# Kernel tuning notes

Measured on AMD Instinct MI355X. Metric: run time of the kernel, lower is better.

Reference implementation:

```python
import jax, jax.numpy as jnp
import numpy as np

B, S, D, H = 4, 1024, 1024, 16
DK = D // H


def setup_inputs() -> dict:
    key = jax.random.key(0)
    ks = jax.random.split(key, 12)
    scale = 1.0 / np.sqrt(D)
    inp = {
        'Q': jax.random.normal(ks[0], (B, S, D), jnp.float32),
        'K': jax.random.normal(ks[1], (B, S, D), jnp.float32),
        'V': jax.random.normal(ks[2], (B, S, D), jnp.float32),
        'mask': jnp.tril(jnp.ones((S, S), bool))[None, None],  # [1,1,S,S] causal
        'Wq': jax.random.normal(ks[3], (D, D), jnp.float32) * scale,
        'bq': jnp.zeros((D,), jnp.float32),
        'Wk': jax.random.normal(ks[4], (D, D), jnp.float32) * scale,
        'bk': jnp.zeros((D,), jnp.float32),
        'Wv': jax.random.normal(ks[5], (D, D), jnp.float32) * scale,
        'bv': jnp.zeros((D,), jnp.float32),
        'Wo': jax.random.normal(ks[6], (D, D), jnp.float32) * scale,
        'bo': jnp.zeros((D,), jnp.float32),
    }
    return inp


def reference(Q, K, V, mask, Wq, bq, Wk, bk, Wv, bv, Wo, bo):
    # Linear projections (torch Linear: x @ W.T + b)
    q = Q @ Wq.T + bq
    k = K @ Wk.T + bk
    v = V @ Wv.T + bv
    # [B,S,D] -> [B,H,S,DK]
    q = q.reshape(B, S, H, DK).transpose(0, 2, 1, 3)
    k = k.reshape(B, S, H, DK).transpose(0, 2, 1, 3)
    v = v.reshape(B, S, H, DK).transpose(0, 2, 1, 3)
    scores = jnp.einsum('bhqd,bhkd->bhqk', q, k) / jnp.sqrt(jnp.float32(DK))
    scores = jnp.where(mask, scores, jnp.float32(-1e9))
    attn = jax.nn.softmax(scores, axis=-1)
    x = jnp.einsum('bhqk,bhkd->bhqd', attn, v)
    x = x.transpose(0, 2, 1, 3).reshape(B, S, D)
    out = x @ Wo.T + bo
    return out, attn
```

## Files before the change

### kernel.cpp

```cpp
#include <hip/hip_runtime.h>
#include <hip/hip_bf16.h>
#include <cstdint>

#define NB 4
#define NS 1024
#define ND 1024
#define NH 16
#define NDK 64
#define NBH 64

typedef unsigned short u16;
typedef __attribute__((ext_vector_type(8))) short short8;
typedef __attribute__((ext_vector_type(4))) float f32x4;
typedef __attribute__((ext_vector_type(4))) unsigned short u16x4;

#define SWZ(r, c) ((c) ^ (((r) & 7) << 3))

__device__ __forceinline__ u16 f2bf(float x) {
  unsigned u = __builtin_bit_cast(unsigned, x);
  return (u16)((u + 0x7fffu + ((u >> 16) & 1u)) >> 16);
}
__device__ __forceinline__ float bf2f(u16 b) {
  return __builtin_bit_cast(float, ((unsigned)b) << 16);
}

__device__ __forceinline__ void async16(u16* lds_dst, const u16* gsrc) {
  __builtin_amdgcn_global_load_lds(
      (const __attribute__((address_space(1))) void*)gsrc,
      (__attribute__((address_space(3))) void*)lds_dst, 16, 0, 0);
}

struct CvtArgs {
  const float* src[7];
  u16* dst[7];
  int n4[7];
};

__global__ __launch_bounds__(256) void cvt_k(CvtArgs a) {
  const int seg = blockIdx.y;
  const float* s = a.src[seg];
  u16* d = a.dst[seg];
  const int n4 = a.n4[seg];
  for (int i = blockIdx.x * 256 + threadIdx.x; i < n4; i += gridDim.x * 256) {
    float4 v = *(const float4*)&s[(size_t)i * 4];
    u16x4 pk = {f2bf(v.x), f2bf(v.y), f2bf(v.z), f2bf(v.w)};
    *(u16x4*)&d[(size_t)i * 4] = pk;
  }
}

template <int KTILES, int LDA, int LDB>
__device__ __forceinline__ void gemm_bt_core(const u16* __restrict__ A,
                                             const u16* __restrict__ BT,
                                             u16* As, u16* Bs, f32x4 (&acc)[4][4],
                                             int bm0, int bn0, int wave, int lane) {
  const int lrow = lane & 15;
  const int lkg = lane >> 4;
  const int wm = wave >> 1, wn = wave & 1;
#pragma unroll 1
  for (int t = 0; t < KTILES; ++t) {
    const int k0 = t * 64;
#pragma unroll
    for (int j = 0; j < 4; ++j) {
      const int c = (wave * 4 + j) * 64 + lane;
      const int row = c >> 3;
      const int gc = (c & 7) ^ (row & 7);
      async16(&As[(wave * 4 + j) * 512], A + (size_t)(bm0 + row) * LDA + k0 + gc * 8);
      async16(&Bs[(wave * 4 + j) * 512], BT + (size_t)(bn0 + row) * LDB + k0 + gc * 8);
    }
    asm volatile("s_waitcnt vmcnt(0)" ::: "memory");
    __syncthreads();
#pragma unroll
    for (int kk = 0; kk < 2; ++kk) {
      short8 av[4], bv[4];
#pragma unroll
      for (int i = 0; i < 4; ++i) {
        const int r = wm * 64 + i * 16 + lrow;
        av[i] = *(const short8*)&As[r * 64 + SWZ(r, kk * 32 + lkg * 8)];
      }
#pragma unroll
      for (int j = 0; j < 4; ++j) {
        const int r = wn * 64 + j * 16 + lrow;
        bv[j] = *(const short8*)&Bs[r * 64 + SWZ(r, kk * 32 + lkg * 8)];
      }
#pragma unroll
      for (int i = 0; i < 4; ++i)
#pragma unroll
        for (int j = 0; j < 4; ++j)
          acc[i][j] = __builtin_amdgcn_mfma_f32_16x16x32_bf16(av[i], bv[j], acc[i][j], 0, 0, 0);
    }
    __syncthreads();
  }
}

struct ProjArgs {
  const u16* A[3];
  const u16* W[3];
  const float* bias[3];
  u16* dst[3];
};

__global__ __launch_bounds__(256, 3) void proj_gemm(ProjArgs pa) {
  const int z = blockIdx.z;
  const u16* A = pa.A[z];
  const u16* BT = pa.W[z];
  const float* bias = pa.bias[z];
  u16* dst = pa.dst[z];

  __shared__ u16 As[128 * 64];
  __shared__ u16 Bs[128 * 64];
  const int tid = threadIdx.x, wave = tid >> 6, lane = tid & 63;
  const int lrow = lane & 15, lkg = lane >> 4;
  const int wm = wave >> 1, wn = wave & 1;
  const int bm0 = blockIdx.x * 128, bn0 = blockIdx.y * 128;

  f32x4 acc[4][4] = {};
  gemm_bt_core<16, ND, ND>(A, BT, As, Bs, acc, bm0, bn0, wave, lane);

#pragma unroll
  for (int i = 0; i < 4; ++i) {
#pragma unroll
    for (int j = 0; j < 4; ++j) {
      const int m0 = bm0 + wm * 64 + i * 16 + lkg * 4;
      const int n = bn0 + wn * 64 + j * 16 + lrow;
      const float bn_ = bias[n];
      const int b = m0 >> 10;
      const int h = n >> 6, dk = n & 63;
      if (z < 2) {
#pragma unroll
        for (int r = 0; r < 4; ++r) {
          const int s = (m0 + r) & 1023;
          dst[(((size_t)(b * NH + h)) * NS + s) * NDK + dk] = f2bf(acc[i][j][r] + bn_);
        }
      } else {
        const int s0 = m0 & 1023;
        u16x4 pk;
#pragma unroll
        for (int r = 0; r < 4; ++r) pk[r] = f2bf(acc[i][j][r] + bn_);
        *(u16x4*)&dst[(((size_t)(b * NH + h)) * NDK + dk) * NS + s0] = pk;
      }
    }
  }
}

__global__ __launch_bounds__(512, 2) void attn_fused(
    const u16* __restrict__ qh, const u16* __restrict__ kh,
    const u16* __restrict__ vT, float* __restrict__ attn,
    u16* __restrict__ xh) {
  __shared__ __align__(16) char smem_raw[81920];
  u16* sc = (u16*)smem_raw;
  u16* kb = (u16*)(smem_raw + 65536);
  float* m_sub = (float*)(smem_raw + 65536);
  float* m_final = (float*)(smem_raw + 65536 + 512);

  const int tid = threadIdx.x;
  const int wave = tid >> 6, lane = tid & 63;
  const int lrow = lane & 15, lkg = lane >> 4;
  const int qs = wave >> 2, ks = wave & 3;

  const int flat = (int)blockIdx.x;
  const int r8 = flat & 7;
  const int inner = flat >> 3;
  const int strip = inner & 31;
  const int bh = r8 + 8 * (inner >> 5);
  const int mt = 31 - strip;

  const int s0 = mt * 32;
  const int nkt = (mt >> 1) + 1;
  const int nk = nkt * 64;
  const u16* Qb = qh + (size_t)bh * NS * NDK;
  const u16* Kb = kh + (size_t)bh * NS * NDK;
  const u16* Vb = vT + (size_t)bh * NS * NDK;
  float* attn_s = attn + (size_t)bh * NS * NS + (size_t)s0 * NS;

  auto stage8k = [&](u16* buf, const u16* src, int ld) {
    const int row = tid >> 3, scol = tid & 7;
    const int gc = scol ^ (row & 7);
    async16(buf + wave * 512, src + (size_t)row * ld + gc * 8);
  };

  if (tid < 256) {
    const int row = tid >> 3, scol = tid & 7;
    const int gc = scol ^ (row & 7);
    async16(kb + 4096 + wave * 512, Qb + (size_t)(s0 + row) * NDK + gc * 8);
  }
  asm volatile("s_waitcnt vmcnt(0)" ::: "memory");
  __syncthreads();
  short8 qv[2];
  {
    const int q = qs * 16 + lrow;
#pragma unroll
    for (int kk = 0; kk < 2; ++kk)
      qv[kk] = *(const short8*)&kb[4096 + q * 64 + SWZ(q, kk * 32 + lkg * 8)];
  }
  __syncthreads();

  float m_run = -3e38f;
  stage8k(kb, Kb, NDK);
#pragma unroll 1
  for (int t = 0; t < nkt; ++t) {
    const bool have_next = (t + 1 < nkt);
    if (have_next) stage8k(kb + ((t + 1) & 1) * 4096, Kb + (size_t)(t + 1) * 64 * NDK, NDK);
    if (have_next) asm volatile("s_waitcnt vmcnt(1)" ::: "memory");
    else           asm volatile("s_waitcnt vmcnt(0)" ::: "memory");
    __builtin_amdgcn_s_barrier();
    const u16* kbuf = kb + (t & 1) * 4096;
    const int krow = ks * 16 + lrow;
    f32x4 acc = {};
#pragma unroll
    for (int kk = 0; kk < 2; ++kk) {
      short8 av = *(const short8*)&kbuf[krow * 64 + SWZ(krow, kk * 32 + lkg * 8)];
      acc = __builtin_amdgcn_mfma_f32_16x16x32_bf16(av, qv[kk], acc, 0, 0, 0);
    }
    const int qloc = qs * 16 + lrow;
    const int qg = s0 + qloc;
    u16x4 pk;
#pragma unroll
    for (int r = 0; r < 4; ++r) {
      float s = acc[r] * 0.125f;
      const int kg = t * 64 + ks * 16 + lkg * 4 + r;
      if (kg > qg) s = -1e30f;
      m_run = fmaxf(m_run, s);
      pk[r] = f2bf(s);
    }
    *(u16x4*)&sc[qloc * 1024 + SWZ(qloc, t * 64 + ks * 16 + lkg * 4)] = pk;
    __builtin_amdgcn_s_barrier();
  }
  __syncthreads();

  m_run = fmaxf(m_run, __shfl_xor(m_run, 16, 64));
  m_run = fmaxf(m_run, __shfl_xor(m_run, 32, 64));
  if (lane < 16) m_sub[wave * 16 + lane] = m_run;
  __syncthreads();
  if (tid < 32) {
    const int qq = tid >> 4, r = tid & 15;
    float m = m_sub[(qq * 4 + 0) * 16 + r];
    m = fmaxf(m, m_sub[(qq * 4 + 1) * 16 + r]);
    m = fmaxf(m, m_sub[(qq * 4 + 2) * 16 + r]);
    m = fmaxf(m, m_sub[(qq * 4 + 3) * 16 + r]);
    m_final[tid] = m;
  }
  __syncthreads();

#pragma unroll 1
  for (int rr = 0; rr < 4; ++rr) {
    const int q = wave * 4 + rr;
    const float m = m_final[q];
    float part = 0.f;
#pragma unroll 1
    for (int c0 = 0; c0 < nk; c0 += 256) {
      const int c = c0 + lane * 4;
      if (c < nk) {
        u16x4 e4 = *(u16x4*)&sc[q * 1024 + SWZ(q, c)];
        u16x4 pk;
#pragma unroll
        for (int e = 0; e < 4; ++e) {
          const float pe = __expf(bf2f(e4[e]) - m);
          part += pe;
          pk[e] = f2bf(pe);
        }
        *(u16x4*)&sc[q * 1024 + SWZ(q, c)] = pk;
      }
    }
#pragma unroll
    for (int o = 32; o; o >>= 1) part += __shfl_xor(part, o, 64);
    const float inv = 1.0f / part;
#pragma unroll 1
    for (int c0 = 0; c0 < NS; c0 += 256) {
      const int c = c0 + lane * 4;
      f32x4 o4 = {0.f, 0.f, 0.f, 0.f};
      if (c < nk) {
        u16x4 e4 = *(u16x4*)&sc[q * 1024 + SWZ(q, c)];
        u16x4 pn;
#pragma unroll
        for (int e = 0; e < 4; ++e) {
          const float pe = bf2f(e4[e]) * inv;
          o4[e] = pe;
          pn[e] = f2bf(pe);
        }
        *(u16x4*)&sc[q * 1024 + SWZ(q, c)] = pn;
      }
      __builtin_nontemporal_store(o4, (f32x4*)&attn_s[(size_t)q * NS + c]);
    }
  }
  __syncthreads();

  f32x4 xacc = {};
  stage8k(kb, Vb, NS);
#pragma unroll 1
  for (int t = 0; t < nkt; ++t) {
    const bool have_next = (t + 1 < nkt);
    if (have_next) stage8k(kb + ((t + 1) & 1) * 4096, Vb + (size_t)(t + 1) * 64, NS);
    if (have_next) asm volatile("s_waitcnt vmcnt(1)" ::: "memory");
    else           asm volatile("s_waitcnt vmcnt(0)" ::: "memory");
    __builtin_amdgcn_s_barrier();
    const u16* vbuf = kb + (t & 1) * 4096;
    const int qrow = qs * 16 + lrow;
    const int vrow = ks * 16 + lrow;
#pragma unroll
    for (int kk = 0; kk < 2; ++kk) {
      short8 av = *(const short8*)&sc[qrow * 1024 + SWZ(qrow, t * 64 + kk * 32 + lkg * 8)];
      short8 bv = *(const short8*)&vbuf[vrow * 64 + SWZ(vrow, kk * 32 + lkg * 8)];
      xacc = __builtin_amdgcn_mfma_f32_16x16x32_bf16(av, bv, xacc, 0, 0, 0);
    }
    __builtin_amdgcn_s_barrier();
  }

  {
    const int b = bh >> 4, h = bh & 15;
    const int dk = ks * 16 + lrow;
#pragma unroll
    for (int r = 0; r < 4; ++r) {
      const int q = qs * 16 + lkg * 4 + r;
      xh[(size_t)(b * NS + s0 + q) * ND + h * NDK + dk] = f2bf(xacc[r]);
    }
  }
}

__global__ __launch_bounds__(256, 3) void out_gemm(const u16* __restrict__ xh,
                                                   const u16* __restrict__ Wo,
                                                   const float* __restrict__ bo,
                                                   float* __restrict__ out) {
  __shared__ u16 As[128 * 64];
  __shared__ u16 Bs[128 * 64];
  const int tid = threadIdx.x, wave = tid >> 6, lane = tid & 63;
  const int lrow = lane & 15, lkg = lane >> 4;
  const int wm = wave >> 1, wn = wave & 1;
  const int bm0 = blockIdx.x * 128, bn0 = blockIdx.y * 128;

  f32x4 acc[4][4] = {};
  gemm_bt_core<16, ND, ND>(xh, Wo, As, Bs, acc, bm0, bn0, wave, lane);

#pragma unroll
  for (int i = 0; i < 4; ++i) {
#pragma unroll
    for (int j = 0; j < 4; ++j) {
      const int m0 = bm0 + wm * 64 + i * 16 + lkg * 4;
      const int n = bn0 + wn * 64 + j * 16 + lrow;
      const float bn_ = bo[n];
#pragma unroll
      for (int r = 0; r < 4; ++r)
        out[(size_t)(m0 + r) * ND + n] = acc[i][j][r] + bn_;
    }
  }
}

extern "C" void kernel_launch(void* const* d_in, const int* in_sizes, int n_in,
                              void* d_out, int out_size, void* d_ws, size_t ws_size,
                              hipStream_t stream) {
  const float* Q = (const float*)d_in[0];
  const float* K = (const float*)d_in[1];
  const float* V = (const float*)d_in[2];
  const float* Wq = (const float*)d_in[4];
  const float* bq = (const float*)d_in[5];
  const float* Wk = (const float*)d_in[6];
  const float* bk = (const float*)d_in[7];
  const float* Wv = (const float*)d_in[8];
  const float* bv = (const float*)d_in[9];
  const float* Wo = (const float*)d_in[10];
  const float* bo = (const float*)d_in[11];

  char* ws = (char*)d_ws;
  const size_t MB = 1u << 20;
  u16* Wq_b = (u16*)(ws + 0 * MB);
  u16* Wk_b = (u16*)(ws + 2 * MB);
  u16* Wv_b = (u16*)(ws + 4 * MB);
  u16* Wo_b = (u16*)(ws + 6 * MB);
  u16* Qb   = (u16*)(ws + 8 * MB);
  u16* Kb   = (u16*)(ws + 16 * MB);
  u16* Vb   = (u16*)(ws + 24 * MB);
  u16* qh   = (u16*)(ws + 32 * MB);
  u16* kh   = (u16*)(ws + 40 * MB);
  u16* vT   = (u16*)(ws + 48 * MB);
  u16* xh   = (u16*)(ws + 56 * MB);

  float* out = (float*)d_out;
  float* attn = out + (size_t)NB * NS * ND;

  CvtArgs ca;
  ca.src[0] = Q;  ca.dst[0] = Qb;   ca.n4[0] = (NB * NS * ND) / 4;
  ca.src[1] = K;  ca.dst[1] = Kb;   ca.n4[1] = (NB * NS * ND) / 4;
  ca.src[2] = V;  ca.dst[2] = Vb;   ca.n4[2] = (NB * NS * ND) / 4;
  ca.src[3] = Wq; ca.dst[3] = Wq_b; ca.n4[3] = (ND * ND) / 4;
  ca.src[4] = Wk; ca.dst[4] = Wk_b; ca.n4[4] = (ND * ND) / 4;
  ca.src[5] = Wv; ca.dst[5] = Wv_b; ca.n4[5] = (ND * ND) / 4;
  ca.src[6] = Wo; ca.dst[6] = Wo_b; ca.n4[6] = (ND * ND) / 4;
  cvt_k<<<dim3(512, 7), 256, 0, stream>>>(ca);

  ProjArgs pa;
  pa.A[0] = Qb; pa.W[0] = Wq_b; pa.bias[0] = bq; pa.dst[0] = qh;
  pa.A[1] = Kb; pa.W[1] = Wk_b; pa.bias[1] = bk; pa.dst[1] = kh;
  pa.A[2] = Vb; pa.W[2] = Wv_b; pa.bias[2] = bv; pa.dst[2] = vT;
  proj_gemm<<<dim3((NB * NS) / 128, ND / 128, 3), 256, 0, stream>>>(pa);

  attn_fused<<<dim3(32 * NBH), 512, 0, stream>>>(qh, kh, vT, attn, xh);

  out_gemm<<<dim3((NB * NS) / 128, ND / 128), 256, 0, stream>>>(xh, Wo_b, bo, out);
}
```

Baseline: 134.1 us.

## Double-buffer output GEMM and defer softmax normalization to the PV epilogue

Adds a double-buffered GEMM core that prefetches the next K tile with async loads while computing the current one, and uses it in the output projection, reducing occupancy to two blocks per CU. In attention, the second softmax pass no longer rewrites normalized probabilities back to shared memory. The unnormalized exponentials feed the P·V MFMA, and the per-row reciprocal is stored in shared memory and applied to the accumulator before the bf16 store. This trades a write pass over the score buffer, plus one extra barrier, for a small rounding difference because bf16 rounding now happens before normalization.

```diff
diff --git a/kernel.cpp b/kernel.cpp
--- a/kernel.cpp
+++ b/kernel.cpp
@@ -92,6 +92,59 @@
   }
 }
 
+template <int KTILES, int LDA, int LDB>
+__device__ __forceinline__ void gemm_bt_db(const u16* __restrict__ A,
+                                           const u16* __restrict__ BT,
+                                           u16 (&As)[2][128 * 64], u16 (&Bs)[2][128 * 64],
+                                           f32x4 (&acc)[4][4],
+                                           int bm0, int bn0, int wave, int lane) {
+  const int lrow = lane & 15;
+  const int lkg = lane >> 4;
+  const int wm = wave >> 1, wn = wave & 1;
+  auto stage = [&](int buf, int t) {
+    const int k0 = t * 64;
+#pragma unroll
+    for (int j = 0; j < 4; ++j) {
+      const int c = (wave * 4 + j) * 64 + lane;
+      const int row = c >> 3;
+      const int gc = (c & 7) ^ (row & 7);
+      async16(&As[buf][(wave * 4 + j) * 512], A + (size_t)(bm0 + row) * LDA + k0 + gc * 8);
+      async16(&Bs[buf][(wave * 4 + j) * 512], BT + (size_t)(bn0 + row) * LDB + k0 + gc * 8);
+    }
+  };
+  stage(0, 0);
+#pragma unroll 1
+  for (int t = 0; t < KTILES; ++t) {
+    const bool have_next = (t + 1 < KTILES);
+    if (have_next) stage((t + 1) & 1, t + 1);
+    if (have_next) asm volatile("s_waitcnt vmcnt(8)" ::: "memory");
+    else           asm volatile("s_waitcnt vmcnt(0)" ::: "memory");
+    __builtin_amdgcn_s_barrier();
+    const u16* as = As[t & 1];
+    const u16* bs = Bs[t & 1];
+#pragma unroll
+    for (int kk = 0; kk < 2; ++kk) {
+      short8 av[4], bv[4];
+#pragma unroll
+      for (int i = 0; i < 4; ++i) {
+        const int r = wm * 64 + i * 16 + lrow;
+        av[i] = *(const short8*)&as[r * 64 + SWZ(r, kk * 32 + lkg * 8)];
+      }
+#pragma unroll
+      for (int j = 0; j < 4; ++j) {
+        const int r = wn * 64 + j * 16 + lrow;
+        bv[j] = *(const short8*)&bs[r * 64 + SWZ(r, kk * 32 + lkg * 8)];
+      }
+#pragma unroll
+      for (int i = 0; i < 4; ++i)
+#pragma unroll
+        for (int j = 0; j < 4; ++j)
+          acc[i][j] = __builtin_amdgcn_mfma_f32_16x16x32_bf16(av[i], bv[j], acc[i][j], 0, 0, 0);
+    }
+    __builtin_amdgcn_s_barrier();
+  }
+}
+
 struct ProjArgs {
   const u16* A[3];
   const u16* W[3];
@@ -151,6 +204,7 @@
   u16* kb = (u16*)(smem_raw + 65536);
   float* m_sub = (float*)(smem_raw + 65536);
   float* m_final = (float*)(smem_raw + 65536 + 512);
+  float* s_inv = (float*)(smem_raw + 65536 + 768);
 
   const int tid = threadIdx.x;
   const int wave = tid >> 6, lane = tid & 63;
@@ -264,24 +318,24 @@
 #pragma unroll
     for (int o = 32; o; o >>= 1) part += __shfl_xor(part, o, 64);
     const float inv = 1.0f / part;
+    if (lane == 0) s_inv[q] = inv;
 #pragma unroll 1
     for (int c0 = 0; c0 < NS; c0 += 256) {
       const int c = c0 + lane * 4;
       f32x4 o4 = {0.f, 0.f, 0.f, 0.f};
       if (c < nk) {
         u16x4 e4 = *(u16x4*)&sc[q * 1024 + SWZ(q, c)];
-        u16x4 pn;
-#pragma unroll
-        for (int e = 0; e < 4; ++e) {
-          const float pe = bf2f(e4[e]) * inv;
-          o4[e] = pe;
-          pn[e] = f2bf(pe);
-        }
-        *(u16x4*)&sc[q * 1024 + SWZ(q, c)] = pn;
+#pragma unroll
+        for (int e = 0; e < 4; ++e) o4[e] = bf2f(e4[e]) * inv;
       }
       __builtin_nontemporal_store(o4, (f32x4*)&attn_s[(size_t)q * NS + c]);
     }
   }
+  __syncthreads();
+
+  f32x4 inv4;
+#pragma unroll
+  for (int r = 0; r < 4; ++r) inv4[r] = s_inv[qs * 16 + lkg * 4 + r];
   __syncthreads();
 
   f32x4 xacc = {};
@@ -311,24 +365,24 @@
 #pragma unroll
     for (int r = 0; r < 4; ++r) {
       const int q = qs * 16 + lkg * 4 + r;
-      xh[(size_t)(b * NS + s0 + q) * ND + h * NDK + dk] = f2bf(xacc[r]);
-    }
-  }
-}
-
-__global__ __launch_bounds__(256, 3) void out_gemm(const u16* __restrict__ xh,
+      xh[(size_t)(b * NS + s0 + q) * ND + h * NDK + dk] = f2bf(xacc[r] * inv4[r]);
+    }
+  }
+}
+
+__global__ __launch_bounds__(256, 2) void out_gemm(const u16* __restrict__ xh,
                                                    const u16* __restrict__ Wo,
                                                    const float* __restrict__ bo,
                                                    float* __restrict__ out) {
-  __shared__ u16 As[128 * 64];
-  __shared__ u16 Bs[128 * 64];
+  __shared__ u16 As[2][128 * 64];
+  __shared__ u16 Bs[2][128 * 64];
   const int tid = threadIdx.x, wave = tid >> 6, lane = tid & 63;
   const int lrow = lane & 15, lkg = lane >> 4;
   const int wm = wave >> 1, wn = wave & 1;
   const int bm0 = blockIdx.x * 128, bn0 = blockIdx.y * 128;
 
   f32x4 acc[4][4] = {};
-  gemm_bt_core<16, ND, ND>(xh, Wo, As, Bs, acc, bm0, bn0, wave, lane);
+  gemm_bt_db<16, ND, ND>(xh, Wo, As, Bs, acc, bm0, bn0, wave, lane);
 
 #pragma unroll
   for (int i = 0; i < 4; ++i) {
```

Measured after the change: 132.6 us (median of 2 runs). Within noise of the previous version (-1.1%).
